# Performance work log

Measured on AMD Instinct MI355X. Metric: run time of the kernel, lower is better.

The kernel has to match this reference:

```python
import jax, jax.numpy as jnp
import numpy as np

WIN_FRONT = 6
WIN_BACK = 3
LN_EPS = 1e-3  # keras LayerNormalization default epsilon

B, T, D = 2, 2048, 512
H, DH = 8, 64  # num_heads, head_size


def chunk_mask(T):
    # Faithful port of _compute_chunk_mask; True = attend allowed.
    i = jnp.arange(T)[:, None]
    j = jnp.arange(T)[None, :]
    low = jnp.maximum(i - WIN_FRONT, 0)
    high = jnp.clip(i + WIN_BACK, 0, T)
    low = low - jnp.maximum(low - T + WIN_BACK, 0)
    high = high + jnp.maximum(WIN_BACK - high, 0)
    return (j >= low) & (j <= high)  # [T, T] bool


def setup_inputs() -> dict:
    key = jax.random.key(0)
    ks = jax.random.split(key, 12)
    s = 0.02
    return {
        "x": jax.random.normal(ks[0], (B, T, D), jnp.float32),
        "gamma": jnp.ones((D,), jnp.float32),
        "beta": jnp.zeros((D,), jnp.float32),
        "Wq": jax.random.normal(ks[1], (D, H, DH), jnp.float32) * s,
        "bq": jnp.zeros((H, DH), jnp.float32),
        "Wk": jax.random.normal(ks[2], (D, H, DH), jnp.float32) * s,
        "bk": jnp.zeros((H, DH), jnp.float32),
        "Wv": jax.random.normal(ks[3], (D, H, DH), jnp.float32) * s,
        "bv": jnp.zeros((H, DH), jnp.float32),
        "Wo": jax.random.normal(ks[4], (H, DH, D), jnp.float32) * s,
        "bo": jnp.zeros((D,), jnp.float32),
    }


def reference(x, gamma, beta, Wq, bq, Wk, bk, Wv, bv, Wo, bo):
    T_ = x.shape[1]
    mask = chunk_mask(T_)  # [T, T] bool, broadcast over batch/heads

    # LayerNorm (eps=1e-3 as keras default)
    mu = jnp.mean(x, axis=-1, keepdims=True)
    var = jnp.var(x, axis=-1, keepdims=True)
    h = (x - mu) * jax.lax.rsqrt(var + LN_EPS) * gamma + beta

    # MultiHeadAttention (keras): q/k/v projections with bias
    q = jnp.einsum('btd,dhk->bthk', h, Wq) + bq
    k = jnp.einsum('bsd,dhk->bshk', h, Wk) + bk
    v = jnp.einsum('bsd,dhk->bshk', h, Wv) + bv

    scores = jnp.einsum('bthk,bshk->bhts', q, k) / jnp.sqrt(jnp.asarray(DH, h.dtype))
    neg = jnp.asarray(-1e9, scores.dtype)
    scores = jnp.where(mask[None, None], scores, neg)
    attn = jax.nn.softmax(scores, axis=-1)

    ctx = jnp.einsum('bhts,bshk->bthk', attn, v)
    out = jnp.einsum('bthk,hkd->btd', ctx, Wo) + bo

    return x + out  # residual add (dropout=0, inference)
```

## Files before the change

### kernel.cpp

```cpp
#include <hip/hip_runtime.h>
#include <hip/hip_bf16.h>

#define B_ 2
#define T_ 2048
#define D_ 512
#define H_ 8
#define DH_ 64
#define NROW 4096
#define NQKV 1536

typedef __bf16 bf16x8 __attribute__((ext_vector_type(8)));
typedef float f32x4 __attribute__((ext_vector_type(4)));

__device__ __forceinline__ unsigned short f2bf(float f) {
  unsigned int u = __float_as_uint(f);
  unsigned int r = (u + 0x7fffu + ((u >> 16) & 1u)) >> 16;
  return (unsigned short)r;
}
__device__ __forceinline__ float bf2f(unsigned short s) {
  return __uint_as_float(((unsigned int)s) << 16);
}

__device__ __forceinline__ void gload_lds16(const void* g, void* l) {
  __builtin_amdgcn_global_load_lds(
      (__attribute__((address_space(1))) void*)(void*)(g),
      (__attribute__((address_space(3))) void*)(l), 16, 0, 0);
}

__global__ __launch_bounds__(256) void prep_ln_kernel(
    const float* __restrict__ Wq, const float* __restrict__ Wk,
    const float* __restrict__ Wv, const float* __restrict__ Wo,
    const float* __restrict__ bq, const float* __restrict__ bk,
    const float* __restrict__ bv,
    const float* __restrict__ x, const float* __restrict__ gamma,
    const float* __restrict__ beta,
    unsigned short* __restrict__ Wt,
    unsigned short* __restrict__ Wot,
    float* __restrict__ bias_cat,
    unsigned short* __restrict__ h)
{
  const int bid = blockIdx.x;
  const int tid = threadIdx.x;
  __shared__ unsigned short tile[64][66];

  if (bid < 256) {
    const int mat = bid >> 6;
    const int tb = bid & 63;
    const int tn = tb >> 3, tk = tb & 7;
    const int k0 = tk << 6, n0 = tn << 6;
    const float* src = (mat == 0) ? Wq : (mat == 1) ? Wk : (mat == 2) ? Wv : Wo;
    unsigned short* dst = (mat < 3) ? (Wt + (size_t)mat * 512 * 512) : Wot;
    #pragma unroll
    for (int p = 0; p < 16; ++p) {
      int e = (p << 8) + tid;
      int kr = e >> 6, nc = e & 63;
      tile[kr][nc] = f2bf(src[(size_t)(k0 + kr) * 512 + n0 + nc]);
    }
    __syncthreads();
    #pragma unroll
    for (int p = 0; p < 16; ++p) {
      int e = (p << 8) + tid;
      int nr = e >> 6, kc = e & 63;
      dst[(size_t)(n0 + nr) * 512 + k0 + kc] = tile[kc][nr];
    }
    return;
  }
  if (bid == 256) {
    for (int i = tid; i < NQKV; i += 256) {
      const float* s = (i < 512) ? bq : ((i < 1024) ? bk : bv);
      bias_cat[i] = s[i & 511];
    }
    return;
  }
  const int lane = tid & 63;
  const int row = ((bid - 257) << 2) + (tid >> 6);
  const float* xr = x + (size_t)row * D_ + lane * 8;
  float4 v0 = *(const float4*)xr;
  float4 v1 = *(const float4*)(xr + 4);
  float xv[8] = {v0.x, v0.y, v0.z, v0.w, v1.x, v1.y, v1.z, v1.w};
  float s = 0.f, ss = 0.f;
  #pragma unroll
  for (int i = 0; i < 8; ++i) { s += xv[i]; ss += xv[i] * xv[i]; }
  #pragma unroll
  for (int off = 32; off > 0; off >>= 1) {
    s  += __shfl_xor(s, off);
    ss += __shfl_xor(ss, off);
  }
  float mu  = s * (1.0f / D_);
  float var = ss * (1.0f / D_) - mu * mu;
  float rs  = rsqrtf(var + 1e-3f);
  const float* gp = gamma + lane * 8;
  const float* bp = beta + lane * 8;
  float4 g0 = *(const float4*)gp;
  float4 g1 = *(const float4*)(gp + 4);
  float4 b0 = *(const float4*)bp;
  float4 b1 = *(const float4*)(bp + 4);
  float gv[8] = {g0.x, g0.y, g0.z, g0.w, g1.x, g1.y, g1.z, g1.w};
  float bv8[8] = {b0.x, b0.y, b0.z, b0.w, b1.x, b1.y, b1.z, b1.w};
  unsigned int pk[4];
  #pragma unroll
  for (int i = 0; i < 4; ++i) {
    unsigned short lo = f2bf((xv[2*i]   - mu) * rs * gv[2*i]   + bv8[2*i]);
    unsigned short hi = f2bf((xv[2*i+1] - mu) * rs * gv[2*i+1] + bv8[2*i+1]);
    pk[i] = (unsigned int)lo | ((unsigned int)hi << 16);
  }
  uint4 out4 = make_uint4(pk[0], pk[1], pk[2], pk[3]);
  *(uint4*)(h + (size_t)row * D_ + lane * 8) = out4;
}

template<int EPI, int BN>
__global__ __launch_bounds__(256) void gemm_bf16(
    const unsigned short* __restrict__ A,
    const unsigned short* __restrict__ Bt,
    const float* __restrict__ bias,
    const float* __restrict__ resid,
    void* __restrict__ outp,
    int M, int N, int K)
{
  constexpr int NF = BN / 32;
  constexpr int WAVE_N = BN / 2;
  __shared__ unsigned short Asm[2][128 * 32];
  __shared__ unsigned short Bsm[2][BN * 32];
  const int tid = threadIdx.x;
  const int lane = tid & 63;
  const int w = tid >> 6;
  const int m0 = blockIdx.y << 7;
  const int n0 = blockIdx.x * BN;
  const int wr = w >> 1, wc = w & 1;

  f32x4 acc[4][NF];
  #pragma unroll
  for (int m = 0; m < 4; ++m)
    #pragma unroll
    for (int n = 0; n < NF; ++n) acc[m][n] = f32x4{0.f, 0.f, 0.f, 0.f};

  const int frow = lane & 15;
  const int fk = (lane >> 4) << 3;

  const int ca0 = (w << 7);
  const int ca1 = ca0 + 64;
  const int c0 = ca0 + lane;
  const int c1 = ca1 + lane;
  const int cb0 = (w << 6) + lane;

  auto stage = [&](int k0, int buf) {
    gload_lds16(A + (size_t)(m0 + (c0 >> 2)) * K + k0 + ((c0 & 3) << 3),
                (char*)Asm[buf] + ca0 * 16);
    gload_lds16(A + (size_t)(m0 + (c1 >> 2)) * K + k0 + ((c1 & 3) << 3),
                (char*)Asm[buf] + ca1 * 16);
    if constexpr (BN == 128) {
      gload_lds16(Bt + (size_t)(n0 + (c0 >> 2)) * K + k0 + ((c0 & 3) << 3),
                  (char*)Bsm[buf] + ca0 * 16);
      gload_lds16(Bt + (size_t)(n0 + (c1 >> 2)) * K + k0 + ((c1 & 3) << 3),
                  (char*)Bsm[buf] + ca1 * 16);
    } else {
      gload_lds16(Bt + (size_t)(n0 + (cb0 >> 2)) * K + k0 + ((cb0 & 3) << 3),
                  (char*)Bsm[buf] + (w << 6) * 16);
    }
  };

  stage(0, 0);
  __syncthreads();

  const int NT = K >> 5;
  for (int t = 0; t < NT; ++t) {
    const int cur = t & 1;
    if (t + 1 < NT) stage((t + 1) << 5, cur ^ 1);
    bf16x8 a[4], b[NF];
    #pragma unroll
    for (int m = 0; m < 4; ++m)
      a[m] = *(const bf16x8*)&Asm[cur][((wr << 6) + (m << 4) + frow) * 32 + fk];
    #pragma unroll
    for (int n = 0; n < NF; ++n)
      b[n] = *(const bf16x8*)&Bsm[cur][(wc * WAVE_N + (n << 4) + frow) * 32 + fk];
    #pragma unroll
    for (int m = 0; m < 4; ++m)
      #pragma unroll
      for (int n = 0; n < NF; ++n)
        acc[m][n] = __builtin_amdgcn_mfma_f32_16x16x32_bf16(a[m], b[n], acc[m][n], 0, 0, 0);
    __syncthreads();
  }

  const int rbase = m0 + (wr << 6) + ((lane >> 4) << 2);
  const int cbase = n0 + wc * WAVE_N + (lane & 15);
  #pragma unroll
  for (int m = 0; m < 4; ++m) {
    #pragma unroll
    for (int n = 0; n < NF; ++n) {
      const int cc = cbase + (n << 4);
      const float bs = bias[cc];
      #pragma unroll
      for (int r = 0; r < 4; ++r) {
        const int rr = rbase + (m << 4) + r;
        const float val = acc[m][n][r] + bs;
        if (EPI == 1) {
          ((unsigned short*)outp)[(size_t)rr * N + cc] = f2bf(val);
        } else {
          const size_t o = (size_t)rr * N + cc;
          ((float*)outp)[o] = val + resid[o];
        }
      }
    }
  }
}

__global__ __launch_bounds__(256) void attn_kernel(
    const unsigned short* __restrict__ qkv,
    unsigned short* __restrict__ ctx)
{
  __shared__ float qs[64][65];
  __shared__ float ks[80][65];
  __shared__ float vs[80][64];
  __shared__ float ssm[64][12];
  __shared__ float ps[64][12];
  const int tid = threadIdx.x;
  const int bx = blockIdx.x;
  const int chunk = bx & 31;
  const int hh = (bx >> 5) & 7;
  const int bb = bx >> 8;
  const int t0 = chunk << 6;
  const size_t base_bt = (size_t)(bb * T_) * NQKV + hh * 64;

  for (int e = tid; e < 64 * 64; e += 256) {
    int i = e >> 6, d = e & 63;
    qs[i][d] = bf2f(qkv[base_bt + (size_t)(t0 + i) * NQKV + d]);
  }
  for (int e = tid; e < 80 * 64; e += 256) {
    int i = e >> 6, d = e & 63;
    int tt = t0 - 6 + i;
    bool ok = (tt >= 0) && (tt < T_);
    if (ok) {
      size_t idx = base_bt + (size_t)tt * NQKV + d;
      ks[i][d] = bf2f(qkv[idx + 512]);
      vs[i][d] = bf2f(qkv[idx + 1024]);
    } else {
      ks[i][d] = 0.f;
      vs[i][d] = 0.f;
    }
  }
  __syncthreads();

  for (int e = tid; e < 640; e += 256) {
    int tl = e / 10, j = e - tl * 10;
    int tk = t0 + tl - 6 + j;
    float sc = -1e30f;
    if (tk >= 0 && tk < T_) {
      float a = 0.f;
      #pragma unroll
      for (int d = 0; d < 64; ++d) a += qs[tl][d] * ks[tl + j][d];
      sc = a * 0.125f;
    }
    ssm[tl][j] = sc;
  }
  __syncthreads();

  if (tid < 64) {
    float mx = -1e30f;
    #pragma unroll
    for (int j = 0; j < 10; ++j) mx = fmaxf(mx, ssm[tid][j]);
    float sum = 0.f;
    float e10[10];
    #pragma unroll
    for (int j = 0; j < 10; ++j) { e10[j] = __expf(ssm[tid][j] - mx); sum += e10[j]; }
    float inv = 1.0f / sum;
    #pragma unroll
    for (int j = 0; j < 10; ++j) ps[tid][j] = e10[j] * inv;
  }
  __syncthreads();

  for (int e = tid; e < 64 * 64; e += 256) {
    int tl = e >> 6, d = e & 63;
    float a = 0.f;
    #pragma unroll
    for (int j = 0; j < 10; ++j) a += ps[tl][j] * vs[tl + j][d];
    ctx[(size_t)(bb * T_ + t0 + tl) * D_ + hh * 64 + d] = f2bf(a);
  }
}

extern "C" void kernel_launch(void* const* d_in, const int* in_sizes, int n_in,
                              void* d_out, int out_size, void* d_ws, size_t ws_size,
                              hipStream_t stream) {
  const float* x     = (const float*)d_in[0];
  const float* gamma = (const float*)d_in[1];
  const float* beta  = (const float*)d_in[2];
  const float* Wq    = (const float*)d_in[3];
  const float* bq    = (const float*)d_in[4];
  const float* Wk    = (const float*)d_in[5];
  const float* bk    = (const float*)d_in[6];
  const float* Wv    = (const float*)d_in[7];
  const float* bv    = (const float*)d_in[8];
  const float* Wo    = (const float*)d_in[9];
  const float* bo    = (const float*)d_in[10];
  float* out = (float*)d_out;

  char* ws = (char*)d_ws;
  unsigned short* h   = (unsigned short*)(ws);
  unsigned short* Wt  = (unsigned short*)(ws + 4194304);
  unsigned short* Wot = (unsigned short*)(ws + 5767168);
  float* bias_cat     = (float*)(ws + 6291456);
  unsigned short* qkv = (unsigned short*)(ws + 6297600);
  unsigned short* ctx = (unsigned short*)(ws + 6297600 + 12582912);

  prep_ln_kernel<<<1281, 256, 0, stream>>>(Wq, Wk, Wv, Wo, bq, bk, bv,
                                           x, gamma, beta, Wt, Wot, bias_cat, h);
  gemm_bf16<1, 64><<<dim3(24, 32), 256, 0, stream>>>(h, Wt, bias_cat, nullptr, qkv, NROW, NQKV, D_);
  attn_kernel<<<512, 256, 0, stream>>>(qkv, ctx);
  gemm_bf16<2, 64><<<dim3(8, 32), 256, 0, stream>>>(ctx, Wot, bo, x, out, NROW, D_, D_);
}
```

Before: 123.9 us.

## Widen GEMM K-tile to 64 with XOR-swizzled LDS; vectorize attention loads

The GEMM now stages K tiles of 64 instead of 32, halving the number of loop iterations and barriers, and uses an XOR swizzle on the LDS layout to avoid bank conflicts when reading MFMA fragments. The attention kernel loads Q/K/V with 16-byte vector loads instead of scalar bf16 loads, and pads the score buffers to 13 columns. LDS use per GEMM block doubles, which could reduce occupancy.

```diff
diff --git a/kernel.cpp b/kernel.cpp
--- a/kernel.cpp
+++ b/kernel.cpp
@@ -108,7 +108,7 @@
   *(uint4*)(h + (size_t)row * D_ + lane * 8) = out4;
 }
 
-template<int EPI, int BN>
+template<int EPI>
 __global__ __launch_bounds__(256) void gemm_bf16(
     const unsigned short* __restrict__ A,
     const unsigned short* __restrict__ Bt,
@@ -117,76 +117,83 @@
     void* __restrict__ outp,
     int M, int N, int K)
 {
-  constexpr int NF = BN / 32;
-  constexpr int WAVE_N = BN / 2;
-  __shared__ unsigned short Asm[2][128 * 32];
-  __shared__ unsigned short Bsm[2][BN * 32];
+  __shared__ unsigned short Asm[2][128 * 64];
+  __shared__ unsigned short Bsm[2][64 * 64];
   const int tid = threadIdx.x;
   const int lane = tid & 63;
   const int w = tid >> 6;
   const int m0 = blockIdx.y << 7;
-  const int n0 = blockIdx.x * BN;
+  const int n0 = blockIdx.x << 6;
   const int wr = w >> 1, wc = w & 1;
 
-  f32x4 acc[4][NF];
+  f32x4 acc[4][2];
   #pragma unroll
   for (int m = 0; m < 4; ++m)
     #pragma unroll
-    for (int n = 0; n < NF; ++n) acc[m][n] = f32x4{0.f, 0.f, 0.f, 0.f};
+    for (int n = 0; n < 2; ++n) acc[m][n] = f32x4{0.f, 0.f, 0.f, 0.f};
 
   const int frow = lane & 15;
-  const int fk = (lane >> 4) << 3;
-
-  const int ca0 = (w << 7);
-  const int ca1 = ca0 + 64;
-  const int c0 = ca0 + lane;
-  const int c1 = ca1 + lane;
-  const int cb0 = (w << 6) + lane;
+  const int fsl = lane >> 4;
 
   auto stage = [&](int k0, int buf) {
-    gload_lds16(A + (size_t)(m0 + (c0 >> 2)) * K + k0 + ((c0 & 3) << 3),
-                (char*)Asm[buf] + ca0 * 16);
-    gload_lds16(A + (size_t)(m0 + (c1 >> 2)) * K + k0 + ((c1 & 3) << 3),
-                (char*)Asm[buf] + ca1 * 16);
-    if constexpr (BN == 128) {
-      gload_lds16(Bt + (size_t)(n0 + (c0 >> 2)) * K + k0 + ((c0 & 3) << 3),
-                  (char*)Bsm[buf] + ca0 * 16);
-      gload_lds16(Bt + (size_t)(n0 + (c1 >> 2)) * K + k0 + ((c1 & 3) << 3),
-                  (char*)Bsm[buf] + ca1 * 16);
-    } else {
-      gload_lds16(Bt + (size_t)(n0 + (cb0 >> 2)) * K + k0 + ((cb0 & 3) << 3),
-                  (char*)Bsm[buf] + (w << 6) * 16);
+    #pragma unroll
+    for (int q = 0; q < 4; ++q) {
+      const int S = (w << 8) + (q << 6) + lane;
+      const int r = S >> 3, g = (S & 7) ^ (r & 7);
+      gload_lds16(A + (size_t)(m0 + r) * K + k0 + (g << 3),
+                  (char*)Asm[buf] + (((w << 8) + (q << 6)) << 4));
+    }
+    #pragma unroll
+    for (int q = 0; q < 2; ++q) {
+      const int S = (w << 7) + (q << 6) + lane;
+      const int r = S >> 3, g = (S & 7) ^ (r & 7);
+      gload_lds16(Bt + (size_t)(n0 + r) * K + k0 + (g << 3),
+                  (char*)Bsm[buf] + (((w << 7) + (q << 6)) << 4));
     }
   };
 
   stage(0, 0);
   __syncthreads();
 
-  const int NT = K >> 5;
+  const int NT = K >> 6;
   for (int t = 0; t < NT; ++t) {
     const int cur = t & 1;
-    if (t + 1 < NT) stage((t + 1) << 5, cur ^ 1);
-    bf16x8 a[4], b[NF];
+    if (t + 1 < NT) stage((t + 1) << 6, cur ^ 1);
+    bf16x8 a[4][2], b[2][2];
+    #pragma unroll
+    for (int m = 0; m < 4; ++m) {
+      const int r = (wr << 6) + (m << 4) + frow;
+      #pragma unroll
+      for (int kk = 0; kk < 2; ++kk) {
+        const int slot = ((kk << 2) + fsl) ^ (r & 7);
+        a[m][kk] = *(const bf16x8*)((char*)Asm[cur] + (r << 7) + (slot << 4));
+      }
+    }
+    #pragma unroll
+    for (int n = 0; n < 2; ++n) {
+      const int r = (wc << 5) + (n << 4) + frow;
+      #pragma unroll
+      for (int kk = 0; kk < 2; ++kk) {
+        const int slot = ((kk << 2) + fsl) ^ (r & 7);
+        b[n][kk] = *(const bf16x8*)((char*)Bsm[cur] + (r << 7) + (slot << 4));
+      }
+    }
     #pragma unroll
     for (int m = 0; m < 4; ++m)
-      a[m] = *(const bf16x8*)&Asm[cur][((wr << 6) + (m << 4) + frow) * 32 + fk];
-    #pragma unroll
-    for (int n = 0; n < NF; ++n)
-      b[n] = *(const bf16x8*)&Bsm[cur][(wc * WAVE_N + (n << 4) + frow) * 32 + fk];
-    #pragma unroll
-    for (int m = 0; m < 4; ++m)
-      #pragma unroll
-      for (int n = 0; n < NF; ++n)
-        acc[m][n] = __builtin_amdgcn_mfma_f32_16x16x32_bf16(a[m], b[n], acc[m][n], 0, 0, 0);
+      #pragma unroll
+      for (int n = 0; n < 2; ++n)
+        #pragma unroll
+        for (int kk = 0; kk < 2; ++kk)
+          acc[m][n] = __builtin_amdgcn_mfma_f32_16x16x32_bf16(a[m][kk], b[n][kk], acc[m][n], 0, 0, 0);
     __syncthreads();
   }
 
   const int rbase = m0 + (wr << 6) + ((lane >> 4) << 2);
-  const int cbase = n0 + wc * WAVE_N + (lane & 15);
+  const int cbase = n0 + (wc << 5) + (lane & 15);
   #pragma unroll
   for (int m = 0; m < 4; ++m) {
     #pragma unroll
-    for (int n = 0; n < NF; ++n) {
+    for (int n = 0; n < 2; ++n) {
       const int cc = cbase + (n << 4);
       const float bs = bias[cc];
       #pragma unroll
@@ -211,8 +218,8 @@
   __shared__ float qs[64][65];
   __shared__ float ks[80][65];
   __shared__ float vs[80][64];
-  __shared__ float ssm[64][12];
-  __shared__ float ps[64][12];
+  __shared__ float ssm[64][13];
+  __shared__ float ps[64][13];
   const int tid = threadIdx.x;
   const int bx = blockIdx.x;
   const int chunk = bx & 31;
@@ -221,21 +228,34 @@
   const int t0 = chunk << 6;
   const size_t base_bt = (size_t)(bb * T_) * NQKV + hh * 64;
 
-  for (int e = tid; e < 64 * 64; e += 256) {
-    int i = e >> 6, d = e & 63;
-    qs[i][d] = bf2f(qkv[base_bt + (size_t)(t0 + i) * NQKV + d]);
-  }
-  for (int e = tid; e < 80 * 64; e += 256) {
-    int i = e >> 6, d = e & 63;
-    int tt = t0 - 6 + i;
-    bool ok = (tt >= 0) && (tt < T_);
-    if (ok) {
-      size_t idx = base_bt + (size_t)tt * NQKV + d;
-      ks[i][d] = bf2f(qkv[idx + 512]);
-      vs[i][d] = bf2f(qkv[idx + 1024]);
+  for (int c = tid; c < 512; c += 256) {
+    int row = c >> 3, grp = c & 7;
+    uint4 u = *(const uint4*)(qkv + base_bt + (size_t)(t0 + row) * NQKV + (grp << 3));
+    float* q8 = &qs[row][grp << 3];
+    unsigned int uu[4] = {u.x, u.y, u.z, u.w};
+    #pragma unroll
+    for (int i = 0; i < 4; ++i) {
+      q8[2*i]   = bf2f((unsigned short)(uu[i] & 0xffff));
+      q8[2*i+1] = bf2f((unsigned short)(uu[i] >> 16));
+    }
+  }
+  for (int c = tid; c < 1280; c += 256) {
+    int kc = (c < 640) ? c : (c - 640);
+    int row = kc >> 3, grp = kc & 7;
+    int tt = t0 - 6 + row;
+    float* d8 = (c < 640) ? &ks[row][grp << 3] : &vs[row][grp << 3];
+    if (tt >= 0 && tt < T_) {
+      size_t idx = base_bt + (size_t)tt * NQKV + (grp << 3) + ((c < 640) ? 512 : 1024);
+      uint4 u = *(const uint4*)(qkv + idx);
+      unsigned int uu[4] = {u.x, u.y, u.z, u.w};
+      #pragma unroll
+      for (int i = 0; i < 4; ++i) {
+        d8[2*i]   = bf2f((unsigned short)(uu[i] & 0xffff));
+        d8[2*i+1] = bf2f((unsigned short)(uu[i] >> 16));
+      }
     } else {
-      ks[i][d] = 0.f;
-      vs[i][d] = 0.f;
+      #pragma unroll
+      for (int i = 0; i < 8; ++i) d8[i] = 0.f;
     }
   }
   __syncthreads();
@@ -303,7 +323,7 @@
 
   prep_ln_kernel<<<1281, 256, 0, stream>>>(Wq, Wk, Wv, Wo, bq, bk, bv,
                                            x, gamma, beta, Wt, Wot, bias_cat, h);
-  gemm_bf16<1, 64><<<dim3(24, 32), 256, 0, stream>>>(h, Wt, bias_cat, nullptr, qkv, NROW, NQKV, D_);
+  gemm_bf16<1><<<dim3(24, 32), 256, 0, stream>>>(h, Wt, bias_cat, nullptr, qkv, NROW, NQKV, D_);
   attn_kernel<<<512, 256, 0, stream>>>(qkv, ctx);
-  gemm_bf16<2, 64><<<dim3(8, 32), 256, 0, stream>>>(ctx, Wot, bo, x, out, NROW, D_, D_);
-}
+  gemm_bf16<2><<<dim3(8, 32), 256, 0, stream>>>(ctx, Wot, bo, x, out, NROW, D_, D_);
+}
```

Result: faster. 116.8 us (-5.7%).
